# Kernel tuning notes

Hardware: AMD Instinct MI355X
Metric: run time of the kernel (lower is better)

The kernel has to match this reference:

```python
import jax, jax.numpy as jnp
import numpy as np

TOP_K = 2

def setup_inputs() -> dict:
    key = jax.random.key(0)
    k1, k2 = jax.random.split(key)
    hidden_states = jax.random.normal(k1, (16384, 4096), dtype=jnp.float32)
    W = jax.random.normal(k2, (64, 4096), dtype=jnp.float32) * 0.02  # classifier weight [num_experts, hidden]
    return {"hidden_states": hidden_states, "W": W}

def reference(hidden_states, W):
    # router logits: [T, E]
    router_logits = jnp.einsum('th,eh->te', hidden_states, W)
    # softmax in float32 (matches dtype=torch.float)
    router_probs = jax.nn.softmax(router_logits.astype(jnp.float32), axis=-1)
    # top-k over experts, then renormalize selected weights
    topk_weight, topk_experts_index = jax.lax.top_k(router_probs, TOP_K)
    topk_weight = topk_weight / jnp.sum(topk_weight, axis=-1, keepdims=True)
    return (topk_weight, router_logits, topk_experts_index)
```

## Files before the change

kernel.cpp:

```cpp
#include <hip/hip_runtime.h>

constexpr int T  = 16384;
constexpr int HD = 4096;
constexpr int E  = 64;
constexpr int BK = 32;
constexpr int NCH = HD / BK;

using short8 = __attribute__((ext_vector_type(8))) short;
using f32x4  = __attribute__((ext_vector_type(4))) float;

#define AS1 __attribute__((address_space(1)))
#define AS3 __attribute__((address_space(3)))

__device__ __forceinline__ unsigned short f2bf(float x) {
  union { float f; unsigned u; } v; v.f = x;
  return (unsigned short)((v.u + 0x7FFFu + ((v.u >> 16) & 1u)) >> 16);
}
__device__ __forceinline__ float bf2f(unsigned short h) {
  union { float f; unsigned u; } v; v.u = ((unsigned)h) << 16;
  return v.f;
}

__device__ __forceinline__ void gload16(const void* g, void* l) {
  __builtin_amdgcn_global_load_lds((const AS1 void*)g, (AS3 void*)l, 16, 0, 0);
}

__global__ __launch_bounds__(256) void wprep(const float* __restrict__ W,
                                             short* __restrict__ img) {
  const int tid = blockIdx.x * 256 + threadIdx.x;
  const int c   = tid >> 9;
  const int rem = tid & 511;
  const int e   = rem >> 3;
  const int sp  = rem & 7;
  const int s   = sp ^ (e & 7);
  const int part = s >> 2;
  const int sl  = s & 3;
  const float* src = W + (size_t)e * HD + c * BK + sl * 8;
  short8 v;
#pragma unroll
  for (int j = 0; j < 8; ++j) {
    float x = src[j];
    unsigned short h = f2bf(x);
    v[j] = part ? (short)f2bf(x - bf2f(h)) : (short)h;
  }
  *(short8*)(img + (size_t)tid * 8) = v;
}

__global__ __launch_bounds__(256) void router_gemm(const float* __restrict__ H,
                                                   const short* __restrict__ wsB,
                                                   float* __restrict__ logits) {
  __shared__ __align__(16) char lds_raw[3 * 8192 + 2 * 8192];

  const int tid  = threadIdx.x;
  const int w    = tid >> 6;
  const int lane = tid & 63;
  const int q    = lane >> 4;
  const int r    = lane & 15;
  const int row0 = blockIdx.x * 64;

  f32x4 acc[4];
#pragma unroll
  for (int ct = 0; ct < 4; ++ct)
#pragma unroll
    for (int i = 0; i < 4; ++i) acc[ct][i] = 0.f;

  auto stageA = [&](int chunk, int abuf) {
    char* dst = lds_raw + abuf * 8192 + w * 2048;
#pragma unroll
    for (int j = 0; j < 2; ++j) {
      const int rl = 8 * j + (lane >> 3);
      const int R  = 16 * w + rl;
      const int s  = (lane & 7) ^ (R & 7);
      const char* src = (const char*)H + ((size_t)(row0 + R) * HD + chunk * BK) * 4 + s * 16;
      gload16(src, dst + j * 1024);
    }
  };
  auto stageB = [&](int chunk, int bbuf) {
    char* dst = lds_raw + 24576 + bbuf * 8192 + w * 2048;
    const char* src = (const char*)wsB + (size_t)chunk * 8192 + w * 2048 + lane * 16;
    gload16(src, dst);
    gload16(src + 1024, dst + 1024);
  };

  const int Rrow = 16 * w + r;
  const int ra   = Rrow & 7;

  auto compute = [&](int abuf, int bbuf) {
    const char* Ar = lds_raw + abuf * 8192 + Rrow * 128;
    const char* Bb = lds_raw + 24576 + bbuf * 8192;
    f32x4 a0 = *(const f32x4*)(Ar + ((2 * q) ^ ra) * 16);
    f32x4 a1 = *(const f32x4*)(Ar + ((2 * q + 1) ^ ra) * 16);
    short8 ahi, alo;
#pragma unroll
    for (int jj = 0; jj < 4; ++jj) {
      unsigned short h0 = f2bf(a0[jj]);
      ahi[jj] = (short)h0; alo[jj] = (short)f2bf(a0[jj] - bf2f(h0));
      unsigned short h1 = f2bf(a1[jj]);
      ahi[4 + jj] = (short)h1; alo[4 + jj] = (short)f2bf(a1[jj] - bf2f(h1));
    }
#pragma unroll
    for (int ct = 0; ct < 4; ++ct) {
      const int e = 16 * ct + r;
      const char* Br = Bb + e * 128;
      short8 bhi = *(const short8*)(Br + ((q) ^ (e & 7)) * 16);
      short8 blo = *(const short8*)(Br + ((4 + q) ^ (e & 7)) * 16);
      acc[ct] = __builtin_amdgcn_mfma_f32_16x16x32_bf16(ahi, bhi, acc[ct], 0, 0, 0);
      acc[ct] = __builtin_amdgcn_mfma_f32_16x16x32_bf16(alo, bhi, acc[ct], 0, 0, 0);
      acc[ct] = __builtin_amdgcn_mfma_f32_16x16x32_bf16(ahi, blo, acc[ct], 0, 0, 0);
    }
  };

  stageA(0, 0);
  stageB(0, 0);
  stageA(1, 1);

  int ab = 0, bb = 0;
  for (int t = 0; t < NCH - 2; ++t) {
    asm volatile("s_waitcnt vmcnt(2)\n\ts_barrier" ::: "memory");
    stageB(t + 1, bb ^ 1);
    int ab2 = ab + 2; if (ab2 >= 3) ab2 -= 3;
    stageA(t + 2, ab2);
    compute(ab, bb);
    ab = (ab == 2) ? 0 : ab + 1;
    bb ^= 1;
  }
  asm volatile("s_waitcnt vmcnt(2)\n\ts_barrier" ::: "memory");
  stageB(NCH - 1, bb ^ 1);
  compute(ab, bb);
  ab = (ab == 2) ? 0 : ab + 1;
  bb ^= 1;
  asm volatile("s_waitcnt vmcnt(0)\n\ts_barrier" ::: "memory");
  compute(ab, bb);

  const int orow = row0 + 16 * w + 4 * q;
#pragma unroll
  for (int ct = 0; ct < 4; ++ct)
#pragma unroll
    for (int rr = 0; rr < 4; ++rr)
      logits[(size_t)(orow + rr) * E + 16 * ct + r] = acc[ct][rr];
}

__global__ __launch_bounds__(256) void router_topk(const float* __restrict__ logits,
                                                   float* __restrict__ topw,
                                                   float* __restrict__ topi) {
  const int tid  = threadIdx.x;
  const int lane = tid & 63;
  const int row  = blockIdx.x * 4 + (tid >> 6);

  const float x = logits[(size_t)row * E + lane];

  float m = x;
#pragma unroll
  for (int off = 32; off; off >>= 1) m = fmaxf(m, __shfl_xor(m, off));
  const float p = expf(x - m);
  float s = p;
#pragma unroll
  for (int off = 32; off; off >>= 1) s += __shfl_xor(s, off);
  const float prob = p / s;

  float v1 = prob; int i1 = lane;
#pragma unroll
  for (int off = 32; off; off >>= 1) {
    const float ov = __shfl_xor(v1, off);
    const int   oi = __shfl_xor(i1, off);
    if (ov > v1 || (ov == v1 && oi < i1)) { v1 = ov; i1 = oi; }
  }
  float v2 = (lane == i1) ? -1.0f : prob; int i2 = lane;
#pragma unroll
  for (int off = 32; off; off >>= 1) {
    const float ov = __shfl_xor(v2, off);
    const int   oi = __shfl_xor(i2, off);
    if (ov > v2 || (ov == v2 && oi < i2)) { v2 = ov; i2 = oi; }
  }

  if (lane == 0) {
    const float sum = v1 + v2;
    topw[(size_t)row * 2 + 0] = v1 / sum;
    topw[(size_t)row * 2 + 1] = v2 / sum;
    topi[(size_t)row * 2 + 0] = (float)i1;
    topi[(size_t)row * 2 + 1] = (float)i2;
  }
}

extern "C" void kernel_launch(void* const* d_in, const int* in_sizes, int n_in,
                              void* d_out, int out_size, void* d_ws, size_t ws_size,
                              hipStream_t stream) {
  const float* H = (const float*)d_in[0];
  const float* W = (const float*)d_in[1];

  float* out    = (float*)d_out;
  float* topw   = out;
  float* logits = out + (size_t)T * 2;
  float* topi   = logits + (size_t)T * E;

  short* wimg = (short*)d_ws;

  wprep<<<256, 256, 0, stream>>>(W, wimg);
  router_gemm<<<T / 64, 256, 0, stream>>>(H, wimg, logits);
  router_topk<<<T / 4, 256, 0, stream>>>(logits, topw, topi);
}
```

Baseline: 83.59 us.

## Fuse top-k into register-pipelined router GEMM and drop LDS staging

Replaces the LDS-staged GEMM (global_load_lds with barriers) with per-wave direct global loads into registers, prefetched several chunks ahead. Top-2 selection is fused into the GEMM epilogue, computed from logits as a two-way softmax, so the separate top-k kernel and its re-read of logits go away. The weight image layout drops its XOR swizzle because LDS is no longer used. The trade-offs are heavy register use (launch bounds 256,1), no sharing of B across waves, and only 256 blocks for the GPU.

```diff
diff --git a/kernel.cpp b/kernel.cpp
--- a/kernel.cpp
+++ b/kernel.cpp
@@ -1,16 +1,13 @@
 #include <hip/hip_runtime.h>
 
-constexpr int T  = 16384;
-constexpr int HD = 4096;
-constexpr int E  = 64;
-constexpr int BK = 32;
+constexpr int T   = 16384;
+constexpr int HD  = 4096;
+constexpr int E   = 64;
+constexpr int BK  = 32;
 constexpr int NCH = HD / BK;
 
 using short8 = __attribute__((ext_vector_type(8))) short;
 using f32x4  = __attribute__((ext_vector_type(4))) float;
-
-#define AS1 __attribute__((address_space(1)))
-#define AS3 __attribute__((address_space(3)))
 
 __device__ __forceinline__ unsigned short f2bf(float x) {
   union { float f; unsigned u; } v; v.f = x;
@@ -21,10 +18,6 @@
   return v.f;
 }
 
-__device__ __forceinline__ void gload16(const void* g, void* l) {
-  __builtin_amdgcn_global_load_lds((const AS1 void*)g, (AS3 void*)l, 16, 0, 0);
-}
-
 __global__ __launch_bounds__(256) void wprep(const float* __restrict__ W,
                                              short* __restrict__ img) {
   const int tid = blockIdx.x * 256 + threadIdx.x;
@@ -32,9 +25,8 @@
   const int rem = tid & 511;
   const int e   = rem >> 3;
   const int sp  = rem & 7;
-  const int s   = sp ^ (e & 7);
-  const int part = s >> 2;
-  const int sl  = s & 3;
+  const int part = sp >> 2;
+  const int sl   = sp & 3;
   const float* src = W + (size_t)e * HD + c * BK + sl * 8;
   short8 v;
 #pragma unroll
@@ -46,139 +38,133 @@
   *(short8*)(img + (size_t)tid * 8) = v;
 }
 
-__global__ __launch_bounds__(256) void router_gemm(const float* __restrict__ H,
-                                                   const short* __restrict__ wsB,
-                                                   float* __restrict__ logits) {
-  __shared__ __align__(16) char lds_raw[3 * 8192 + 2 * 8192];
-
-  const int tid  = threadIdx.x;
-  const int w    = tid >> 6;
-  const int lane = tid & 63;
+__global__ __launch_bounds__(256, 1) void router_gemm(
+    const float* __restrict__ H, const short* __restrict__ img,
+    float* __restrict__ logits, float* __restrict__ topw, float* __restrict__ topi) {
+  const int w    = threadIdx.x >> 6;
+  const int lane = threadIdx.x & 63;
   const int q    = lane >> 4;
   const int r    = lane & 15;
-  const int row0 = blockIdx.x * 64;
+  const int gw   = blockIdx.x * 4 + w;
 
-  f32x4 acc[4];
+  const float* pA = H + (size_t)(gw * 16 + r) * HD + q * 8;
+  const short* pB = img + r * 64 + q * 8;
+
+  f32x4  Ab[4][2];
+  short8 Bh[2][4], Bl[2][4];
+  f32x4  acc[4];
 #pragma unroll
   for (int ct = 0; ct < 4; ++ct)
 #pragma unroll
     for (int i = 0; i < 4; ++i) acc[ct][i] = 0.f;
 
-  auto stageA = [&](int chunk, int abuf) {
-    char* dst = lds_raw + abuf * 8192 + w * 2048;
+  auto cvt = [&](f32x4 a0, f32x4 a1, short8& hi, short8& lo) {
 #pragma unroll
-    for (int j = 0; j < 2; ++j) {
-      const int rl = 8 * j + (lane >> 3);
-      const int R  = 16 * w + rl;
-      const int s  = (lane & 7) ^ (R & 7);
-      const char* src = (const char*)H + ((size_t)(row0 + R) * HD + chunk * BK) * 4 + s * 16;
-      gload16(src, dst + j * 1024);
-    }
-  };
-  auto stageB = [&](int chunk, int bbuf) {
-    char* dst = lds_raw + 24576 + bbuf * 8192 + w * 2048;
-    const char* src = (const char*)wsB + (size_t)chunk * 8192 + w * 2048 + lane * 16;
-    gload16(src, dst);
-    gload16(src + 1024, dst + 1024);
-  };
-
-  const int Rrow = 16 * w + r;
-  const int ra   = Rrow & 7;
-
-  auto compute = [&](int abuf, int bbuf) {
-    const char* Ar = lds_raw + abuf * 8192 + Rrow * 128;
-    const char* Bb = lds_raw + 24576 + bbuf * 8192;
-    f32x4 a0 = *(const f32x4*)(Ar + ((2 * q) ^ ra) * 16);
-    f32x4 a1 = *(const f32x4*)(Ar + ((2 * q + 1) ^ ra) * 16);
-    short8 ahi, alo;
-#pragma unroll
-    for (int jj = 0; jj < 4; ++jj) {
-      unsigned short h0 = f2bf(a0[jj]);
-      ahi[jj] = (short)h0; alo[jj] = (short)f2bf(a0[jj] - bf2f(h0));
-      unsigned short h1 = f2bf(a1[jj]);
-      ahi[4 + jj] = (short)h1; alo[4 + jj] = (short)f2bf(a1[jj] - bf2f(h1));
-    }
-#pragma unroll
-    for (int ct = 0; ct < 4; ++ct) {
-      const int e = 16 * ct + r;
-      const char* Br = Bb + e * 128;
-      short8 bhi = *(const short8*)(Br + ((q) ^ (e & 7)) * 16);
-      short8 blo = *(const short8*)(Br + ((4 + q) ^ (e & 7)) * 16);
-      acc[ct] = __builtin_amdgcn_mfma_f32_16x16x32_bf16(ahi, bhi, acc[ct], 0, 0, 0);
-      acc[ct] = __builtin_amdgcn_mfma_f32_16x16x32_bf16(alo, bhi, acc[ct], 0, 0, 0);
-      acc[ct] = __builtin_amdgcn_mfma_f32_16x16x32_bf16(ahi, blo, acc[ct], 0, 0, 0);
+    for (int j = 0; j < 4; ++j) {
+      unsigned short h0 = f2bf(a0[j]);
+      hi[j] = (short)h0; lo[j] = (short)f2bf(a0[j] - bf2f(h0));
+      unsigned short h1 = f2bf(a1[j]);
+      hi[4 + j] = (short)h1; lo[4 + j] = (short)f2bf(a1[j] - bf2f(h1));
     }
   };
 
-  stageA(0, 0);
-  stageB(0, 0);
-  stageA(1, 1);
+#pragma unroll
+  for (int i = 0; i < 4; ++i) {
+    Ab[i][0] = *(const f32x4*)(pA + i * BK);
+    Ab[i][1] = *(const f32x4*)(pA + i * BK + 4);
+  }
+#pragma unroll
+  for (int i = 0; i < 2; ++i)
+#pragma unroll
+    for (int ct = 0; ct < 4; ++ct) {
+      Bh[i][ct] = *(const short8*)(pB + ct * 1024 + (size_t)i * 4096);
+      Bl[i][ct] = *(const short8*)(pB + ct * 1024 + (size_t)i * 4096 + 32);
+    }
 
-  int ab = 0, bb = 0;
-  for (int t = 0; t < NCH - 2; ++t) {
-    asm volatile("s_waitcnt vmcnt(2)\n\ts_barrier" ::: "memory");
-    stageB(t + 1, bb ^ 1);
-    int ab2 = ab + 2; if (ab2 >= 3) ab2 -= 3;
-    stageA(t + 2, ab2);
-    compute(ab, bb);
-    ab = (ab == 2) ? 0 : ab + 1;
-    bb ^= 1;
+#define GEMM_BODY(U, TT, PREA, PREB)                                            \
+  {                                                                             \
+    f32x4 a0 = Ab[U][0], a1 = Ab[U][1];                                         \
+    short8 bh0 = Bh[(U)&1][0], bh1 = Bh[(U)&1][1],                              \
+           bh2 = Bh[(U)&1][2], bh3 = Bh[(U)&1][3];                              \
+    short8 bl0 = Bl[(U)&1][0], bl1 = Bl[(U)&1][1],                              \
+           bl2 = Bl[(U)&1][2], bl3 = Bl[(U)&1][3];                              \
+    if (PREA) {                                                                 \
+      Ab[U][0] = *(const f32x4*)(pA + ((TT) + 4) * BK);                         \
+      Ab[U][1] = *(const f32x4*)(pA + ((TT) + 4) * BK + 4);                     \
+    }                                                                           \
+    if (PREB) {                                                                 \
+      _Pragma("unroll")                                                         \
+      for (int ct = 0; ct < 4; ++ct) {                                          \
+        Bh[(U)&1][ct] = *(const short8*)(pB + ct * 1024 + (size_t)((TT) + 2) * 4096);      \
+        Bl[(U)&1][ct] = *(const short8*)(pB + ct * 1024 + (size_t)((TT) + 2) * 4096 + 32); \
+      }                                                                         \
+    }                                                                           \
+    short8 ahi, alo;                                                            \
+    cvt(a0, a1, ahi, alo);                                                      \
+    acc[0] = __builtin_amdgcn_mfma_f32_16x16x32_bf16(ahi, bh0, acc[0], 0, 0, 0);\
+    acc[0] = __builtin_amdgcn_mfma_f32_16x16x32_bf16(alo, bh0, acc[0], 0, 0, 0);\
+    acc[0] = __builtin_amdgcn_mfma_f32_16x16x32_bf16(ahi, bl0, acc[0], 0, 0, 0);\
+    acc[1] = __builtin_amdgcn_mfma_f32_16x16x32_bf16(ahi, bh1, acc[1], 0, 0, 0);\
+    acc[1] = __builtin_amdgcn_mfma_f32_16x16x32_bf16(alo, bh1, acc[1], 0, 0, 0);\
+    acc[1] = __builtin_amdgcn_mfma_f32_16x16x32_bf16(ahi, bl1, acc[1], 0, 0, 0);\
+    acc[2] = __builtin_amdgcn_mfma_f32_16x16x32_bf16(ahi, bh2, acc[2], 0, 0, 0);\
+    acc[2] = __builtin_amdgcn_mfma_f32_16x16x32_bf16(alo, bh2, acc[2], 0, 0, 0);\
+    acc[2] = __builtin_amdgcn_mfma_f32_16x16x32_bf16(ahi, bl2, acc[2], 0, 0, 0);\
+    acc[3] = __builtin_amdgcn_mfma_f32_16x16x32_bf16(ahi, bh3, acc[3], 0, 0, 0);\
+    acc[3] = __builtin_amdgcn_mfma_f32_16x16x32_bf16(alo, bh3, acc[3], 0, 0, 0);\
+    acc[3] = __builtin_amdgcn_mfma_f32_16x16x32_bf16(ahi, bl3, acc[3], 0, 0, 0);\
   }
-  asm volatile("s_waitcnt vmcnt(2)\n\ts_barrier" ::: "memory");
-  stageB(NCH - 1, bb ^ 1);
-  compute(ab, bb);
-  ab = (ab == 2) ? 0 : ab + 1;
-  bb ^= 1;
-  asm volatile("s_waitcnt vmcnt(0)\n\ts_barrier" ::: "memory");
-  compute(ab, bb);
 
-  const int orow = row0 + 16 * w + 4 * q;
+  for (int t0 = 0; t0 <= NCH - 8; t0 += 4) {
+    GEMM_BODY(0, t0 + 0, true, true)
+    GEMM_BODY(1, t0 + 1, true, true)
+    GEMM_BODY(2, t0 + 2, true, true)
+    GEMM_BODY(3, t0 + 3, true, true)
+  }
+  GEMM_BODY(0, 124, false, true)
+  GEMM_BODY(1, 125, false, true)
+  GEMM_BODY(2, 126, false, false)
+  GEMM_BODY(3, 127, false, false)
+#undef GEMM_BODY
+
+  const int orow = gw * 16 + 4 * q;
 #pragma unroll
   for (int ct = 0; ct < 4; ++ct)
 #pragma unroll
     for (int rr = 0; rr < 4; ++rr)
       logits[(size_t)(orow + rr) * E + 16 * ct + r] = acc[ct][rr];
-}
 
-__global__ __launch_bounds__(256) void router_topk(const float* __restrict__ logits,
-                                                   float* __restrict__ topw,
-                                                   float* __restrict__ topi) {
-  const int tid  = threadIdx.x;
-  const int lane = tid & 63;
-  const int row  = blockIdx.x * 4 + (tid >> 6);
-
-  const float x = logits[(size_t)row * E + lane];
-
-  float m = x;
 #pragma unroll
-  for (int off = 32; off; off >>= 1) m = fmaxf(m, __shfl_xor(m, off));
-  const float p = expf(x - m);
-  float s = p;
+  for (int rr = 0; rr < 4; ++rr) {
+    float v1 = acc[0][rr]; int i1 = r;
+    { float x = acc[1][rr]; if (x > v1) { v1 = x; i1 = 16 + r; } }
+    { float x = acc[2][rr]; if (x > v1) { v1 = x; i1 = 32 + r; } }
+    { float x = acc[3][rr]; if (x > v1) { v1 = x; i1 = 48 + r; } }
 #pragma unroll
-  for (int off = 32; off; off >>= 1) s += __shfl_xor(s, off);
-  const float prob = p / s;
-
-  float v1 = prob; int i1 = lane;
+    for (int off = 1; off < 16; off <<= 1) {
+      float ov = __shfl_xor(v1, off); int oi = __shfl_xor(i1, off);
+      if (ov > v1 || (ov == v1 && oi < i1)) { v1 = ov; i1 = oi; }
+    }
+    float v2 = -3.4e38f; int i2 = 0;
 #pragma unroll
-  for (int off = 32; off; off >>= 1) {
-    const float ov = __shfl_xor(v1, off);
-    const int   oi = __shfl_xor(i1, off);
-    if (ov > v1 || (ov == v1 && oi < i1)) { v1 = ov; i1 = oi; }
-  }
-  float v2 = (lane == i1) ? -1.0f : prob; int i2 = lane;
+    for (int ct = 0; ct < 4; ++ct) {
+      int idx = 16 * ct + r; float x = acc[ct][rr];
+      if (idx != i1 && x > v2) { v2 = x; i2 = idx; }
+    }
 #pragma unroll
-  for (int off = 32; off; off >>= 1) {
-    const float ov = __shfl_xor(v2, off);
-    const int   oi = __shfl_xor(i2, off);
-    if (ov > v2 || (ov == v2 && oi < i2)) { v2 = ov; i2 = oi; }
-  }
-
-  if (lane == 0) {
-    const float sum = v1 + v2;
-    topw[(size_t)row * 2 + 0] = v1 / sum;
-    topw[(size_t)row * 2 + 1] = v2 / sum;
-    topi[(size_t)row * 2 + 0] = (float)i1;
-    topi[(size_t)row * 2 + 1] = (float)i2;
+    for (int off = 1; off < 16; off <<= 1) {
+      float ov = __shfl_xor(v2, off); int oi = __shfl_xor(i2, off);
+      if (ov > v2 || (ov == v2 && oi < i2)) { v2 = ov; i2 = oi; }
+    }
+    if (r == 0) {
+      float d  = __expf(v2 - v1);
+      float w1 = 1.0f / (1.0f + d);
+      const int R = orow + rr;
+      topw[(size_t)R * 2 + 0] = w1;
+      topw[(size_t)R * 2 + 1] = 1.0f - w1;
+      topi[(size_t)R * 2 + 0] = (float)i1;
+      topi[(size_t)R * 2 + 1] = (float)i2;
+    }
   }
 }
 
@@ -196,6 +182,5 @@
   short* wimg = (short*)d_ws;
 
   wprep<<<256, 256, 0, stream>>>(W, wimg);
-  router_gemm<<<T / 64, 256, 0, stream>>>(H, wimg, logits);
-  router_topk<<<T / 4, 256, 0, stream>>>(logits, topw, topi);
+  router_gemm<<<256, 256, 0, stream>>>(H, wimg, logits, topw, topi);
 }
```

Result: slower. 155.4 us (+85.9%).
